# Performance work log

Hardware: AMD Instinct MI355X
Metric: run time of the kernel (lower is better)

The kernel has to match this reference:

```python
import jax, jax.numpy as jnp
import numpy as np

N_EMBD = 768
HEAD_SIZE = 64
B, T = 32, 1024


def setup_inputs() -> dict:
    key = jax.random.key(0)
    k1, k2, k3, k4 = jax.random.split(key, 4)
    x = jax.random.normal(k1, (B, T, N_EMBD), dtype=jnp.float32)
    Wq = jax.random.normal(k2, (N_EMBD, HEAD_SIZE), dtype=jnp.float32) * 0.02
    Wk = jax.random.normal(k3, (N_EMBD, HEAD_SIZE), dtype=jnp.float32) * 0.02
    Wv = jax.random.normal(k4, (N_EMBD, HEAD_SIZE), dtype=jnp.float32) * 0.02
    return {"x": x, "Wq": Wq, "Wk": Wk, "Wv": Wv}


def _apply_rope(q, k):
    # q, k: [B, T, D]; interleaved (even/odd) RoPE exactly as the torch source
    seq_len, dim = q.shape[-2], q.shape[-1]
    pos = jnp.arange(seq_len, dtype=jnp.float32)[:, None]                      # [T, 1]
    div_term = jnp.exp(jnp.arange(0, dim, 2, dtype=jnp.float32) * (-jnp.log(10000.0) / dim))  # [D/2]
    sin_emb = jnp.sin(pos * div_term)                                          # [T, D/2]
    cos_emb = jnp.cos(pos * div_term)                                          # [T, D/2]

    def rot(t):
        te, to = t[..., ::2], t[..., 1::2]
        re = te * cos_emb - to * sin_emb
        ro = te * sin_emb + to * cos_emb
        # interleave back: [..., T, D/2, 2] -> [..., T, D]
        return jnp.stack([re, ro], axis=-1).reshape(t.shape)

    return rot(q), rot(k)


def reference(x, Wq, Wk, Wv):
    Bx, Tx, C = x.shape  # C == n_embd
    q = x @ Wq  # [B, T, D]
    k = x @ Wk
    v = x @ Wv
    q, k = _apply_rope(q, k)
    # NOTE: source scales by C**-0.5 where C = n_embd, not head_size
    wei = jnp.einsum('btd,bsd->bts', q, k) * (C ** -0.5)  # [B, T, T]
    causal = jnp.tril(jnp.ones((Tx, Tx), dtype=bool))
    wei = jnp.where(causal, wei, -jnp.inf)
    wei = jax.nn.softmax(wei, axis=-1)
    # dropout is identity in eval mode
    out = jnp.einsum('bts,bsd->btd', wei, v)  # [B, T, D]
    return out
```

## Files before the change

### kernel.cpp

```cpp
#include <hip/hip_runtime.h>
#include <cmath>

#define B 32
#define T 1024
#define CDIM 768
#define D 64
#define SCALE 0.03608439182435161f
#define XSTR 72

typedef short bf16x8 __attribute__((ext_vector_type(8)));
typedef float f32x4 __attribute__((ext_vector_type(4)));
typedef unsigned short u16x8 __attribute__((ext_vector_type(8)));

__device__ inline ushort f2bf(float f) {
  union { float f; unsigned u; } v{f};
  unsigned r = (v.u + 0x7FFFu + ((v.u >> 16) & 1u)) >> 16;
  return (ushort)r;
}

__global__ __launch_bounds__(256) void wt_prep(
    const float* __restrict__ Wq, const float* __restrict__ Wk,
    const float* __restrict__ Wv, ushort* __restrict__ Wt)
{
  const int n   = blockIdx.x;
  const int sel = n >> 6, col = n & 63;
  const float* W = (sel == 0) ? Wq : (sel == 1) ? Wk : Wv;
  const float sc = (sel == 0) ? SCALE : 1.f;
  for (int k = threadIdx.x; k < CDIM; k += 256)
    Wt[(size_t)n * CDIM + k] = f2bf(W[(size_t)k * D + col] * sc);
}

__global__ __launch_bounds__(256) void proj_mfma(
    const float* __restrict__ x,
    const ushort* __restrict__ Wt,
    ushort* __restrict__ qkv)
{
  const int t    = threadIdx.x;
  const int lane = t & 63;
  const int wid  = t >> 6;
  const int ln16 = lane & 15;
  const int quad = lane >> 4;
  const int row0 = blockIdx.x * 64;

  __shared__ ushort Xs[2][64 * XSTR];
  __shared__ ushort Ws[2][192 * XSTR];

  f32x4 acc[12];
  #pragma unroll
  for (int nt = 0; nt < 12; ++nt) acc[nt] = (f32x4){0.f, 0.f, 0.f, 0.f};

  float4 xp[2][4];
  u16x8  wp[2][6];

  auto load_stage = [&](int s, int set) {
    const int k0 = s * 64;
    #pragma unroll
    for (int it = 0; it < 4; ++it) {
      int slot = it * 256 + t, row = slot >> 4, kq = slot & 15;
      xp[set][it] = *(const float4*)(x + (size_t)(row0 + row) * CDIM + k0 + kq * 4);
    }
    #pragma unroll
    for (int it = 0; it < 6; ++it) {
      int slot = it * 256 + t, n = slot >> 3, kb = slot & 7;
      wp[set][it] = *(const u16x8*)(Wt + (size_t)n * CDIM + k0 + kb * 8);
    }
  };

  load_stage(0, 0);
  load_stage(1, 1);
  int buf = 0;
  for (int s = 0; s < CDIM / 64; ++s) {
    const int set = s & 1;
    #pragma unroll
    for (int it = 0; it < 4; ++it) {
      int slot = it * 256 + t, row = slot >> 4, kq = slot & 15;
      ushort4 bv;
      bv.x = f2bf(xp[set][it].x); bv.y = f2bf(xp[set][it].y);
      bv.z = f2bf(xp[set][it].z); bv.w = f2bf(xp[set][it].w);
      *(ushort4*)&Xs[buf][row * XSTR + kq * 4] = bv;
    }
    #pragma unroll
    for (int it = 0; it < 6; ++it) {
      int slot = it * 256 + t, n = slot >> 3, kb = slot & 7;
      *(u16x8*)&Ws[buf][n * XSTR + kb * 8] = wp[set][it];
    }
    __syncthreads();
    if (s + 2 < CDIM / 64) load_stage(s + 2, set);

    #pragma unroll
    for (int ks = 0; ks < 2; ++ks) {
      bf16x8 a = *(const bf16x8*)&Xs[buf][(wid * 16 + ln16) * XSTR + ks * 32 + quad * 8];
      #pragma unroll
      for (int nt = 0; nt < 12; ++nt) {
        bf16x8 bb = *(const bf16x8*)&Ws[buf][(nt * 16 + ln16) * XSTR + ks * 32 + quad * 8];
        acc[nt] = __builtin_amdgcn_mfma_f32_16x16x32_bf16(a, bb, acc[nt], 0, 0, 0);
      }
    }
    buf ^= 1;
  }

  #pragma unroll
  for (int nt = 0; nt < 12; ++nt) {
    const int sel = nt >> 2;
    const int d   = (nt & 3) * 16 + ln16;
    ushort* outb = qkv + (size_t)sel * (B * T * D);
    if (sel < 2) {
      const float freq = __expf((float)(d & 62) * (-0.14391156855801f));
      const float sgn  = (d & 1) ? 1.f : -1.f;
      #pragma unroll
      for (int reg = 0; reg < 4; ++reg) {
        int rowg = row0 + wid * 16 + quad * 4 + reg;
        float s, c;
        __sincosf((float)(rowg & (T - 1)) * freq, &s, &c);
        float val = acc[nt][reg];
        float partner = __shfl_xor(val, 1, 64);
        outb[(size_t)rowg * D + d] = f2bf(fmaf(sgn * partner, s, val * c));
      }
    } else {
      #pragma unroll
      for (int reg = 0; reg < 4; ++reg) {
        int rowg = row0 + wid * 16 + quad * 4 + reg;
        outb[(size_t)rowg * D + d] = f2bf(acc[nt][reg]);
      }
    }
  }
}

__global__ __launch_bounds__(256) void attn_mfma(
    const ushort* __restrict__ qg,
    const ushort* __restrict__ kg,
    const ushort* __restrict__ vg,
    float* __restrict__ out)
{
  const int t    = threadIdx.x;
  const int lane = t & 63;
  const int wid  = t >> 6;
  const int ln16 = lane & 15;
  const int quad = lane >> 4;
  const int qt   = 15 - (int)blockIdx.x;
  const int b    = blockIdx.y;

  __shared__ ushort Ks[2][64 * XSTR];
  __shared__ ushort Vt[2][64 * XSTR];
  __shared__ ushort Pl[64 * XSTR];

  bf16x8 qf[2];
  {
    const ushort* qrow = qg + (size_t)(b * T + qt * 64 + wid * 16 + ln16) * D;
    qf[0] = *(const bf16x8*)(qrow + quad * 8);
    qf[1] = *(const bf16x8*)(qrow + quad * 8 + 32);
  }

  f32x4 O[4];
  #pragma unroll
  for (int nt = 0; nt < 4; ++nt) O[nt] = (f32x4){0.f, 0.f, 0.f, 0.f};
  float l = 0.f;

  const int kb = t & 15, db = t >> 4;
  const int d0 = db * 4, kk0 = kb * 4;

  u16x8  kp[2];
  ushort4 vp[4];
  auto load_kv = [&](int kt) {
    #pragma unroll
    for (int i = 0; i < 2; ++i) {
      int slot = i * 256 + t, row = slot >> 3, dblk = slot & 7;
      kp[i] = *(const u16x8*)(kg + (size_t)(b * T + kt * 64 + row) * D + dblk * 8);
    }
    #pragma unroll
    for (int i = 0; i < 4; ++i)
      vp[i] = *(const ushort4*)(vg + (size_t)(b * T + kt * 64 + kk0 + i) * D + d0);
  };

  load_kv(0);
  int buf = 0;
  for (int kt = 0; kt <= qt; ++kt) {
    #pragma unroll
    for (int i = 0; i < 2; ++i) {
      int slot = i * 256 + t, row = slot >> 3, dblk = slot & 7;
      *(u16x8*)&Ks[buf][row * XSTR + dblk * 8] = kp[i];
    }
    const ushort* vpe = (const ushort*)vp;
    #pragma unroll
    for (int j = 0; j < 4; ++j) {
      ushort4 c;
      c.x = vpe[0 * 4 + j]; c.y = vpe[1 * 4 + j];
      c.z = vpe[2 * 4 + j]; c.w = vpe[3 * 4 + j];
      *(ushort4*)&Vt[buf][(d0 + j) * XSTR + kk0] = c;
    }
    __syncthreads();
    if (kt < qt) load_kv(kt + 1);

    f32x4 s[4];
    #pragma unroll
    for (int mt = 0; mt < 4; ++mt) s[mt] = (f32x4){0.f, 0.f, 0.f, 0.f};
    #pragma unroll
    for (int ks = 0; ks < 2; ++ks)
      #pragma unroll
      for (int mt = 0; mt < 4; ++mt) {
        bf16x8 kf = *(const bf16x8*)&Ks[buf][(mt * 16 + ln16) * XSTR + quad * 8 + ks * 32];
        s[mt] = __builtin_amdgcn_mfma_f32_16x16x32_bf16(kf, qf[ks], s[mt], 0, 0, 0);
      }

    if (kt == qt) {
      const int ql = wid * 16 + ln16;
      #pragma unroll
      for (int mt = 0; mt < 4; ++mt)
        #pragma unroll
        for (int reg = 0; reg < 4; ++reg)
          if (mt * 16 + quad * 4 + reg > ql) s[mt][reg] = -1e30f;
    }

    float psum = 0.f;
    #pragma unroll
    for (int mt = 0; mt < 4; ++mt) {
      float p0 = __expf(s[mt][0]), p1 = __expf(s[mt][1]);
      float p2 = __expf(s[mt][2]), p3 = __expf(s[mt][3]);
      psum += (p0 + p1) + (p2 + p3);
      ushort4 pk;
      pk.x = f2bf(p0); pk.y = f2bf(p1); pk.z = f2bf(p2); pk.w = f2bf(p3);
      *(ushort4*)&Pl[(wid * 16 + ln16) * XSTR + mt * 16 + quad * 4] = pk;
    }
    psum += __shfl_xor(psum, 16, 64);
    psum += __shfl_xor(psum, 32, 64);
    l += psum;

    bf16x8 pa[2];
    pa[0] = *(const bf16x8*)&Pl[(wid * 16 + ln16) * XSTR + quad * 8];
    pa[1] = *(const bf16x8*)&Pl[(wid * 16 + ln16) * XSTR + quad * 8 + 32];
    #pragma unroll
    for (int ks = 0; ks < 2; ++ks)
      #pragma unroll
      for (int nt = 0; nt < 4; ++nt) {
        bf16x8 vf = *(const bf16x8*)&Vt[buf][(nt * 16 + ln16) * XSTR + quad * 8 + ks * 32];
        O[nt] = __builtin_amdgcn_mfma_f32_16x16x32_bf16(pa[ks], vf, O[nt], 0, 0, 0);
      }
    buf ^= 1;
  }

  float inv = 1.f / l;
  #pragma unroll
  for (int reg = 0; reg < 4; ++reg) {
    float iv = __shfl(inv, quad * 4 + reg, 64);
    size_t row = (size_t)(b * T + qt * 64 + wid * 16 + quad * 4 + reg) * D;
    #pragma unroll
    for (int nt = 0; nt < 4; ++nt)
      out[row + nt * 16 + ln16] = O[nt][reg] * iv;
  }
}

extern "C" void kernel_launch(void* const* d_in, const int* in_sizes, int n_in,
                              void* d_out, int out_size, void* d_ws, size_t ws_size,
                              hipStream_t stream) {
  const float* x  = (const float*)d_in[0];
  const float* Wq = (const float*)d_in[1];
  const float* Wk = (const float*)d_in[2];
  const float* Wv = (const float*)d_in[3];
  float* outp = (float*)d_out;

  ushort* qkv = (ushort*)d_ws;
  ushort* Wt  = qkv + (size_t)3 * B * T * D;

  wt_prep<<<dim3(192), dim3(256), 0, stream>>>(Wq, Wk, Wv, Wt);
  proj_mfma<<<dim3((B * T) / 64), dim3(256), 0, stream>>>(x, Wt, qkv);
  attn_mfma<<<dim3(T / 64, B), dim3(256), 0, stream>>>(
      qkv, qkv + (size_t)B * T * D, qkv + 2 * (size_t)B * T * D, outp);
}
```

Baseline: 183.3 us.

## Split attention over key chunks with a reduce pass, and split projection columns

The attention kernel now splits each query tile's causal key range into chunks of up to four key tiles. A constant lookup table pairs long and short chunks so the work per block is more even. Each block writes unnormalized partial outputs and row sums to the workspace, and a new reduce kernel adds them up and normalizes. The projection kernel is also split into two column halves per row tile, with a higher occupancy hint, to give it more blocks. The cost is extra global traffic: the partial buffers are written and read back, and x is read twice by the projection.

Result: slower. 208.9 us (+14.0%).

```diff
diff --git a/kernel.cpp b/kernel.cpp
--- a/kernel.cpp
+++ b/kernel.cpp
@@ -17,6 +17,13 @@
   unsigned r = (v.u + 0x7FFFu + ((v.u >> 16) & 1u)) >> 16;
   return (ushort)r;
 }
+
+__constant__ int qt_tab[40] = {15,15,15,15, 14,14,14, 13,13,13, 12,12,12,
+                               11,11,11, 10,10, 9,9, 8,8, 7,7, 6, 5, 4, 3,
+                               14,10,6,2, 13,9,5,1, 12,8,4,0};
+__constant__ int ch_tab[40] = {0,1,2,3, 0,1,2, 0,1,2, 0,1,2,
+                               0,1,2, 0,1, 0,1, 0,1, 0,1, 0, 0, 0, 0,
+                               3,2,1,0, 3,2,1,0, 3,2,1,0};
 
 __global__ __launch_bounds__(256) void wt_prep(
     const float* __restrict__ Wq, const float* __restrict__ Wk,
@@ -30,7 +37,7 @@
     Wt[(size_t)n * CDIM + k] = f2bf(W[(size_t)k * D + col] * sc);
 }
 
-__global__ __launch_bounds__(256) void proj_mfma(
+__global__ __launch_bounds__(256, 3) void proj_mfma(
     const float* __restrict__ x,
     const ushort* __restrict__ Wt,
     ushort* __restrict__ qkv)
@@ -41,16 +48,17 @@
   const int ln16 = lane & 15;
   const int quad = lane >> 4;
   const int row0 = blockIdx.x * 64;
+  const int n0   = blockIdx.y * 96;
 
   __shared__ ushort Xs[2][64 * XSTR];
-  __shared__ ushort Ws[2][192 * XSTR];
-
-  f32x4 acc[12];
-  #pragma unroll
-  for (int nt = 0; nt < 12; ++nt) acc[nt] = (f32x4){0.f, 0.f, 0.f, 0.f};
+  __shared__ ushort Ws[2][96 * XSTR];
+
+  f32x4 acc[6];
+  #pragma unroll
+  for (int nt = 0; nt < 6; ++nt) acc[nt] = (f32x4){0.f, 0.f, 0.f, 0.f};
 
   float4 xp[2][4];
-  u16x8  wp[2][6];
+  u16x8  wp[2][3];
 
   auto load_stage = [&](int s, int set) {
     const int k0 = s * 64;
@@ -60,9 +68,9 @@
       xp[set][it] = *(const float4*)(x + (size_t)(row0 + row) * CDIM + k0 + kq * 4);
     }
     #pragma unroll
-    for (int it = 0; it < 6; ++it) {
-      int slot = it * 256 + t, n = slot >> 3, kb = slot & 7;
-      wp[set][it] = *(const u16x8*)(Wt + (size_t)n * CDIM + k0 + kb * 8);
+    for (int it = 0; it < 3; ++it) {
+      int slot = it * 256 + t, nl = slot >> 3, kb = slot & 7;
+      wp[set][it] = *(const u16x8*)(Wt + (size_t)(n0 + nl) * CDIM + k0 + kb * 8);
     }
   };
 
@@ -80,9 +88,9 @@
       *(ushort4*)&Xs[buf][row * XSTR + kq * 4] = bv;
     }
     #pragma unroll
-    for (int it = 0; it < 6; ++it) {
-      int slot = it * 256 + t, n = slot >> 3, kb = slot & 7;
-      *(u16x8*)&Ws[buf][n * XSTR + kb * 8] = wp[set][it];
+    for (int it = 0; it < 3; ++it) {
+      int slot = it * 256 + t, nl = slot >> 3, kb = slot & 7;
+      *(u16x8*)&Ws[buf][nl * XSTR + kb * 8] = wp[set][it];
     }
     __syncthreads();
     if (s + 2 < CDIM / 64) load_stage(s + 2, set);
@@ -91,7 +99,7 @@
     for (int ks = 0; ks < 2; ++ks) {
       bf16x8 a = *(const bf16x8*)&Xs[buf][(wid * 16 + ln16) * XSTR + ks * 32 + quad * 8];
       #pragma unroll
-      for (int nt = 0; nt < 12; ++nt) {
+      for (int nt = 0; nt < 6; ++nt) {
         bf16x8 bb = *(const bf16x8*)&Ws[buf][(nt * 16 + ln16) * XSTR + ks * 32 + quad * 8];
         acc[nt] = __builtin_amdgcn_mfma_f32_16x16x32_bf16(a, bb, acc[nt], 0, 0, 0);
       }
@@ -100,9 +108,10 @@
   }
 
   #pragma unroll
-  for (int nt = 0; nt < 12; ++nt) {
-    const int sel = nt >> 2;
-    const int d   = (nt & 3) * 16 + ln16;
+  for (int nt = 0; nt < 6; ++nt) {
+    const int n   = n0 + nt * 16 + ln16;
+    const int sel = n >> 6;
+    const int d   = n & 63;
     ushort* outb = qkv + (size_t)sel * (B * T * D);
     if (sel < 2) {
       const float freq = __expf((float)(d & 62) * (-0.14391156855801f));
@@ -126,19 +135,23 @@
   }
 }
 
-__global__ __launch_bounds__(256) void attn_mfma(
+__global__ __launch_bounds__(256, 3) void attn_part(
     const ushort* __restrict__ qg,
     const ushort* __restrict__ kg,
     const ushort* __restrict__ vg,
-    float* __restrict__ out)
+    float* __restrict__ pO,
+    float* __restrict__ pl)
 {
   const int t    = threadIdx.x;
   const int lane = t & 63;
   const int wid  = t >> 6;
   const int ln16 = lane & 15;
   const int quad = lane >> 4;
-  const int qt   = 15 - (int)blockIdx.x;
+  const int qt   = qt_tab[blockIdx.x];
+  const int ch   = ch_tab[blockIdx.x];
   const int b    = blockIdx.y;
+  const int kt0  = ch * 4;
+  const int kend = min(kt0 + 3, qt);
 
   __shared__ ushort Ks[2][64 * XSTR];
   __shared__ ushort Vt[2][64 * XSTR];
@@ -172,9 +185,9 @@
       vp[i] = *(const ushort4*)(vg + (size_t)(b * T + kt * 64 + kk0 + i) * D + d0);
   };
 
-  load_kv(0);
+  load_kv(kt0);
   int buf = 0;
-  for (int kt = 0; kt <= qt; ++kt) {
+  for (int kt = kt0; kt <= kend; ++kt) {
     #pragma unroll
     for (int i = 0; i < 2; ++i) {
       int slot = i * 256 + t, row = slot >> 3, dblk = slot & 7;
@@ -189,7 +202,7 @@
       *(ushort4*)&Vt[buf][(d0 + j) * XSTR + kk0] = c;
     }
     __syncthreads();
-    if (kt < qt) load_kv(kt + 1);
+    if (kt < kend) load_kv(kt + 1);
 
     f32x4 s[4];
     #pragma unroll
@@ -238,14 +251,43 @@
     buf ^= 1;
   }
 
-  float inv = 1.f / l;
+  float* po = pO + ((size_t)(b * 16 + qt) * 4 + ch) * 4096;
   #pragma unroll
   for (int reg = 0; reg < 4; ++reg) {
-    float iv = __shfl(inv, quad * 4 + reg, 64);
-    size_t row = (size_t)(b * T + qt * 64 + wid * 16 + quad * 4 + reg) * D;
+    int q = wid * 16 + quad * 4 + reg;
     #pragma unroll
     for (int nt = 0; nt < 4; ++nt)
-      out[row + nt * 16 + ln16] = O[nt][reg] * iv;
+      po[q * 64 + nt * 16 + ln16] = O[nt][reg];
+  }
+  if (quad == 0)
+    pl[((size_t)(b * 16 + qt) * 4 + ch) * 64 + wid * 16 + ln16] = l;
+}
+
+__global__ __launch_bounds__(256) void attn_reduce(
+    const float* __restrict__ pO,
+    const float* __restrict__ pl,
+    float* __restrict__ out)
+{
+  const int qt = blockIdx.x, b = blockIdx.y;
+  const int t  = threadIdx.x;
+  const int nc = qt / 4 + 1;
+  const size_t base = (size_t)(b * 16 + qt) * 4;
+
+  __shared__ float linv[64];
+  if (t < 64) {
+    float s = 0.f;
+    for (int c = 0; c < nc; ++c) s += pl[(base + c) * 64 + t];
+    linv[t] = 1.f / s;
+  }
+  __syncthreads();
+
+  float* ob = out + ((size_t)b * T + qt * 64) * D;
+  #pragma unroll
+  for (int i = 0; i < 16; ++i) {
+    int idx = i * 256 + t;
+    float s = 0.f;
+    for (int c = 0; c < nc; ++c) s += pO[(base + c) * 4096 + idx];
+    ob[idx] = s * linv[idx >> 6];
   }
 }
 
@@ -260,9 +302,12 @@
 
   ushort* qkv = (ushort*)d_ws;
   ushort* Wt  = qkv + (size_t)3 * B * T * D;
+  float*  pO  = (float*)(Wt + (size_t)192 * CDIM);
+  float*  pl  = pO + (size_t)B * 16 * 4 * 4096;
 
   wt_prep<<<dim3(192), dim3(256), 0, stream>>>(Wq, Wk, Wv, Wt);
-  proj_mfma<<<dim3((B * T) / 64), dim3(256), 0, stream>>>(x, Wt, qkv);
-  attn_mfma<<<dim3(T / 64, B), dim3(256), 0, stream>>>(
-      qkv, qkv + (size_t)B * T * D, qkv + 2 * (size_t)B * T * D, outp);
-}
+  proj_mfma<<<dim3((B * T) / 64, 2), dim3(256), 0, stream>>>(x, Wt, qkv);
+  attn_part<<<dim3(40, B), dim3(256), 0, stream>>>(
+      qkv, qkv + (size_t)B * T * D, qkv + 2 * (size_t)B * T * D, pO, pl);
+  attn_reduce<<<dim3(16, B), dim3(256), 0, stream>>>(pO, pl, outp);
+}
```
